# Optimization experiments

Hardware: AMD Instinct MI355X
Metric: run time of the kernel (lower is better)

## Reference

```python
import jax, jax.numpy as jnp
import numpy as np

N, E = 100000, 1600000
IN_C, HID, OUT_C, EDGE_D, GRAPH_D = 32, 32, 8, 16, 16

def _lin_w(key, fan_in, fan_out):
    return jax.random.normal(key, (fan_in, fan_out), dtype=jnp.float32) * (1.0 / np.sqrt(fan_in))

def setup_inputs() -> dict:
    key = jax.random.key(0)
    ks = jax.random.split(key, 12)
    return {
        "x": jax.random.uniform(ks[0], (N, IN_C), dtype=jnp.float32),
        "edge_attr": jax.random.uniform(ks[1], (E, EDGE_D), dtype=jnp.float32),
        "graph_attr": jax.random.uniform(ks[2], (1, GRAPH_D), dtype=jnp.float32),
        "edge_index": jax.random.randint(ks[3], (2, E), 0, N, dtype=jnp.int32),
        "batch": jnp.zeros((N,), dtype=jnp.int32),
        "W_node": _lin_w(ks[4], IN_C, HID),
        "b_node": jnp.zeros((HID,), jnp.float32),
        "W_graph": _lin_w(ks[5], GRAPH_D, GRAPH_D),
        "b_graph": jnp.zeros((GRAPH_D,), jnp.float32),
        "W_edge_agg": _lin_w(ks[6], 2 * HID + EDGE_D + GRAPH_D, EDGE_D),
        "b_edge_agg": jnp.zeros((EDGE_D,), jnp.float32),
        "W_node_agg": _lin_w(ks[7], EDGE_D + HID + GRAPH_D, HID),
        "b_node_agg": jnp.zeros((HID,), jnp.float32),
        "W_sage_l": _lin_w(ks[8], HID, OUT_C),
        "b_sage_l": jnp.zeros((OUT_C,), jnp.float32),
        "W_sage_r": _lin_w(ks[9], HID, OUT_C),
    }

def _seg_mean(vals, idx, num_segments):
    # scatter-mean: sum per segment / count (count clamped to 1 for empty segments)
    sums = jax.ops.segment_sum(vals, idx, num_segments=num_segments)
    cnt = jax.ops.segment_sum(jnp.ones((vals.shape[0],), vals.dtype), idx, num_segments=num_segments)
    return sums / jnp.maximum(cnt, 1.0)[:, None]

def reference(x, edge_attr, graph_attr, edge_index, batch,
              W_node, b_node, W_graph, b_graph,
              W_edge_agg, b_edge_agg, W_node_agg, b_node_agg,
              W_sage_l, b_sage_l, W_sage_r):
    n = x.shape[0]
    row, col = edge_index[0], edge_index[1]
    # node / graph embeddings (plain linear, no activation)
    h_i = x @ W_node + b_node                       # [N, HID]
    h_G = graph_attr @ W_graph + b_graph            # [1, GRAPH_D]
    h_G_e = jnp.broadcast_to(h_G, (row.shape[0], h_G.shape[1]))
    # edge aggregator: gather both endpoints, concat, linear, relu
    edge_in = jnp.concatenate([h_i[row], h_i[col], edge_attr, h_G_e], axis=-1)  # [E, 96]
    h_edge_agg = jax.nn.relu(edge_in @ W_edge_agg + b_edge_agg)                 # [E, EDGE_D]
    # per-node mean of edges whose source == node (replaces O(N*E) python loop)
    m_N = _seg_mean(h_edge_agg, row, n)             # [N, EDGE_D]
    # node aggregator
    h_G_n = jnp.broadcast_to(h_G, (n, h_G.shape[1]))
    h_i2 = jax.nn.relu(jnp.concatenate([h_i, m_N, h_G_n], axis=-1) @ W_node_agg + b_node_agg)
    # SAGEConv (mean aggr): out = lin_l(mean_{j->i} x_j) + lin_r(x_i)
    agg = _seg_mean(h_i2[row], col, n)
    h_nodes = agg @ W_sage_l + b_sage_l + h_i2 @ W_sage_r  # [N, OUT_C]
    # global mean pool over batch assignment (single graph here)
    pooled = _seg_mean(h_nodes, batch, 1)           # [1, OUT_C]
    return jax.nn.log_softmax(pooled, axis=1)
```

## Files before the change

### kernel.cpp

```cpp
#include <hip/hip_runtime.h>
#include <hip/hip_fp16.h>
#include <hip/hip_fp8.h>

#define HID 32
#define IN_C 32
#define EDGE_D 16
#define GRAPH_D 16
#define OUT_C 8
#define STRIDE 48

__device__ __forceinline__ unsigned char f32_to_fp8(float f) {
    __hip_fp8_e4m3 v(f);
    return (unsigned char)v.__x;
}
__device__ __forceinline__ float fp8_to_f32(unsigned char b) {
    __hip_fp8_e4m3 v;
    v.__x = (__hip_fp8_storage_t)b;
    return (float)v;
}

__global__ void __launch_bounds__(256)
k_node_emb(const float* __restrict__ x,
           const float* __restrict__ W,
           const float* __restrict__ b,
           const float* __restrict__ graph_attr,
           const float* __restrict__ W_graph,
           const float* __restrict__ b_graph,
           const float* __restrict__ W_edge_agg,
           const float* __restrict__ b_edge_agg,
           const float* __restrict__ W_node_agg,
           const float* __restrict__ b_node_agg,
           float* __restrict__ bias_edge,
           float* __restrict__ bias_node,
           int* __restrict__ zero_base, int zero_count,
           __half* __restrict__ h,
           unsigned char* __restrict__ Pr,
           unsigned char* __restrict__ Pc, int n) {
    __shared__ float hG[GRAPH_D];
    int t = threadIdx.x;
    for (int idx = blockIdx.x * blockDim.x + t; idx < zero_count;
         idx += gridDim.x * blockDim.x)
        zero_base[idx] = 0;

    if (blockIdx.x == 0 && t < GRAPH_D) {
        float acc = b_graph[t];
        for (int d = 0; d < GRAPH_D; d++)
            acc += graph_attr[d] * W_graph[d * GRAPH_D + t];
        hG[t] = acc;
    }
    __syncthreads();
    if (blockIdx.x == 0) {
        if (t < EDGE_D) {
            float acc = b_edge_agg[t];
            for (int d = 0; d < GRAPH_D; d++)
                acc += hG[d] * W_edge_agg[(2 * HID + EDGE_D + d) * EDGE_D + t];
            bias_edge[t] = acc;
        }
        if (t < HID) {
            float acc = b_node_agg[t];
            for (int d = 0; d < GRAPH_D; d++)
                acc += hG[d] * W_node_agg[(HID + EDGE_D + d) * HID + t];
            bias_node[t] = acc;
        }
    }

    int i = blockIdx.x * blockDim.x + t;
    if (i >= n) return;
    float in[IN_C];
    const float4* xr = (const float4*)(x + (size_t)i * IN_C);
#pragma unroll
    for (int q = 0; q < IN_C / 4; q++) {
        float4 v = xr[q];
        in[4 * q + 0] = v.x; in[4 * q + 1] = v.y;
        in[4 * q + 2] = v.z; in[4 * q + 3] = v.w;
    }
    float acc[HID];
#pragma unroll
    for (int j = 0; j < HID; j++) acc[j] = b[j];
#pragma unroll
    for (int k = 0; k < IN_C; k++) {
        float a = in[k];
#pragma unroll
        for (int j = 0; j < HID; j++) acc[j] += a * W[k * HID + j];
    }
    float4 packed[4];
    __half2* ph = (__half2*)packed;
#pragma unroll
    for (int j = 0; j < 16; j++)
        ph[j] = __floats2half2_rn(acc[2 * j], acc[2 * j + 1]);
    float4* hr = (float4*)(h + (size_t)i * HID);
#pragma unroll
    for (int q = 0; q < 4; q++) hr[q] = packed[q];

    float pr[EDGE_D], pc[EDGE_D];
#pragma unroll
    for (int j = 0; j < EDGE_D; j++) { pr[j] = 0.f; pc[j] = 0.f; }
#pragma unroll
    for (int k = 0; k < HID; k++) {
        float a = acc[k];
#pragma unroll
        for (int j = 0; j < EDGE_D; j++) {
            pr[j] += a * W_edge_agg[k * EDGE_D + j];
            pc[j] += a * W_edge_agg[(HID + k) * EDGE_D + j];
        }
    }
    unsigned char pb[EDGE_D];
#pragma unroll
    for (int j = 0; j < EDGE_D; j++) pb[j] = f32_to_fp8(pr[j]);
    *(uint4*)(Pr + (size_t)i * EDGE_D) = *(const uint4*)pb;
#pragma unroll
    for (int j = 0; j < EDGE_D; j++) pb[j] = f32_to_fp8(pc[j]);
    *(uint4*)(Pc + (size_t)i * EDGE_D) = *(const uint4*)pb;
}

__global__ void __launch_bounds__(256)
k_edge_place(const int* __restrict__ ei,
             const unsigned char* __restrict__ Pr,
             const unsigned char* __restrict__ Pc,
             const float* __restrict__ ea,
             const float* __restrict__ We,
             const float* __restrict__ biasE,
             int* __restrict__ cur_row,
             int* __restrict__ cur_col,
             __half* __restrict__ he_bucket, int E) {
    int e = blockIdx.x * blockDim.x + threadIdx.x;
    if (e >= E) return;
    int r = ei[e];
    int c = ei[E + e];

    uint4 g = *(const uint4*)(Pr + (size_t)r * EDGE_D);
    uint4 q = *(const uint4*)(Pc + (size_t)c * EDGE_D);
    float eav[EDGE_D];
    {
        const float4* er = (const float4*)(ea + (size_t)e * EDGE_D);
#pragma unroll
        for (int k = 0; k < 4; k++) {
            float4 v = er[k];
            eav[4 * k + 0] = v.x; eav[4 * k + 1] = v.y;
            eav[4 * k + 2] = v.z; eav[4 * k + 3] = v.w;
        }
    }
    int pr = atomicAdd(cur_row + r, 1);
    atomicAdd(cur_col + c, 1);

    float acc[EDGE_D];
    {
        const unsigned char* gb = (const unsigned char*)&g;
        const unsigned char* qb = (const unsigned char*)&q;
#pragma unroll
        for (int j = 0; j < EDGE_D; j++)
            acc[j] = biasE[j] + fp8_to_f32(gb[j]) + fp8_to_f32(qb[j]);
    }
#pragma unroll
    for (int k = 0; k < EDGE_D; k++) {
        float a = eav[k];
#pragma unroll
        for (int j = 0; j < EDGE_D; j++)
            acc[j] += a * We[(2 * HID + k) * EDGE_D + j];
    }

    if (pr < STRIDE) {
        float4 packed[2];
        __half2* ph = (__half2*)packed;
#pragma unroll
        for (int j = 0; j < 8; j++)
            ph[j] = __floats2half2_rn(fmaxf(acc[2 * j], 0.f),
                                      fmaxf(acc[2 * j + 1], 0.f));
        float4* dst = (float4*)(he_bucket + ((size_t)r * STRIDE + pr) * EDGE_D);
        dst[0] = packed[0];
        dst[1] = packed[1];
    }
}

#define RNODES 128
__global__ void __launch_bounds__(256)
k_reduce(const __half* __restrict__ hi,
         const __half* __restrict__ he_bucket,
         const int* __restrict__ cur_row,
         const int* __restrict__ batch,
         const float* __restrict__ Wna,
         const float* __restrict__ Wsl,
         const float* __restrict__ Wsr,
         const float* __restrict__ biasN,
         __half* __restrict__ zout,
         float* __restrict__ pool,
         float* __restrict__ ncnt, int n) {
    __shared__ float ms_s[RNODES][EDGE_D + 1];
    __shared__ int cnt_s[RNODES];
    __shared__ float red[4][OUT_C + 1];
    __shared__ float redc[4];
    int tid = threadIdx.x;
    int g = tid >> 4;
    int l = tid & 15;
    int base = blockIdx.x * RNODES;

    if (tid < RNODES)
        cnt_s[tid] = (base + tid < n) ? cur_row[base + tid] : 0;
    __syncthreads();

    for (int iter = 0; iter < RNODES / 16; iter++) {
        int node = base + iter * 16 + g;
        int cnt = cnt_s[iter * 16 + g];
        int d = cnt < STRIDE ? cnt : STRIDE;
        float inv = 1.0f / fmaxf((float)cnt, 1.0f);
        float a16[EDGE_D];
#pragma unroll
        for (int j = 0; j < EDGE_D; j++) a16[j] = 0.f;
        const __half* bb = he_bucket + (size_t)node * STRIDE * EDGE_D;
        for (int t = l; t < d; t += 16) {
            const float4* rp = (const float4*)(bb + t * EDGE_D);
            float4 lo = rp[0], hi4 = rp[1];
            const __half2* hp0 = (const __half2*)&lo;
            const __half2* hp1 = (const __half2*)&hi4;
#pragma unroll
            for (int j = 0; j < 4; j++) {
                float2 f0 = __half22float2(hp0[j]);
                float2 f1 = __half22float2(hp1[j]);
                a16[2 * j]     += f0.x; a16[2 * j + 1] += f0.y;
                a16[8 + 2 * j] += f1.x; a16[8 + 2 * j + 1] += f1.y;
            }
        }
#pragma unroll
        for (int m = 8; m >= 1; m >>= 1) {
#pragma unroll
            for (int k = 0; k < m; k++) {
                float send = (l & m) ? a16[k] : a16[k + m];
                float recv = __shfl_xor(send, m, 16);
                float keep = (l & m) ? a16[k + m] : a16[k];
                a16[k] = keep + recv;
            }
        }
        ms_s[iter * 16 + g][l] = a16[0] * inv;
    }
    __syncthreads();

    int i = base + tid;
    float rvv[OUT_C];
#pragma unroll
    for (int j = 0; j < OUT_C; j++) rvv[j] = 0.f;
    float cc = 0.f;

    if (tid < RNODES && i < n) {
        float ms[EDGE_D];
#pragma unroll
        for (int k = 0; k < EDGE_D; k++) ms[k] = ms_s[tid][k];

        float hr[HID];
        {
            float4 t[4];
            const float4* hrow = (const float4*)(hi + (size_t)i * HID);
#pragma unroll
            for (int q = 0; q < 4; q++) t[q] = hrow[q];
            const __half2* hp = (const __half2*)t;
#pragma unroll
            for (int j = 0; j < 16; j++) {
                float2 f = __half22float2(hp[j]);
                hr[2 * j] = f.x; hr[2 * j + 1] = f.y;
            }
        }
        float h2[HID];
#pragma unroll
        for (int j = 0; j < HID; j++) h2[j] = biasN[j];
#pragma unroll
        for (int k = 0; k < HID; k++) {
            float a = hr[k];
#pragma unroll
            for (int j = 0; j < HID; j++) h2[j] += a * Wna[k * HID + j];
        }
#pragma unroll
        for (int k = 0; k < EDGE_D; k++) {
            float a = ms[k];
#pragma unroll
            for (int j = 0; j < HID; j++) h2[j] += a * Wna[(HID + k) * HID + j];
        }
#pragma unroll
        for (int j = 0; j < HID; j++) h2[j] = fmaxf(h2[j], 0.f);

        float zv[OUT_C];
#pragma unroll
        for (int j = 0; j < OUT_C; j++) zv[j] = 0.f;
#pragma unroll
        for (int k = 0; k < HID; k++) {
            float a = h2[k];
#pragma unroll
            for (int j = 0; j < OUT_C; j++) {
                zv[j]  += a * Wsl[k * OUT_C + j];
                rvv[j] += a * Wsr[k * OUT_C + j];
            }
        }
        float4 packed;
        __half2* ph = (__half2*)&packed;
#pragma unroll
        for (int j = 0; j < 4; j++)
            ph[j] = __floats2half2_rn(zv[2 * j], zv[2 * j + 1]);
        *(float4*)(zout + (size_t)i * OUT_C) = packed;
        if (batch[i] == 0) cc = 1.f; else {
#pragma unroll
            for (int j = 0; j < OUT_C; j++) rvv[j] = 0.f;
        }
    }
#pragma unroll
    for (int off = 32; off > 0; off >>= 1) {
#pragma unroll
        for (int j = 0; j < OUT_C; j++) rvv[j] += __shfl_down(rvv[j], off, 64);
        cc += __shfl_down(cc, off, 64);
    }
    int w = tid >> 6;
    if ((tid & 63) == 0) {
#pragma unroll
        for (int j = 0; j < OUT_C; j++) red[w][j] = rvv[j];
        redc[w] = cc;
    }
    __syncthreads();
    if (tid < OUT_C) {
        float s = red[0][tid] + red[1][tid] + red[2][tid] + red[3][tid];
        atomicAdd(pool + tid, s);
    }
    if (tid == OUT_C) {
        atomicAdd(ncnt, redc[0] + redc[1] + redc[2] + redc[3]);
    }
}

#define POOL_BLOCKS 1280
__global__ void __launch_bounds__(256)
k_pool(const int* __restrict__ ei,
       const __half* __restrict__ z,
       const int* __restrict__ cur_col,
       float* __restrict__ pool, int E) {
    __shared__ float red[4][OUT_C + 1];
    int tid = threadIdx.x;
    float w8[OUT_C];
#pragma unroll
    for (int j = 0; j < OUT_C; j++) w8[j] = 0.f;
    for (int e = blockIdx.x * blockDim.x + tid; e < E;
         e += gridDim.x * blockDim.x) {
        int r = ei[e];
        int c = ei[E + e];
        float inv = 1.0f / fmaxf((float)cur_col[c], 1.0f);
        float4 t = *(const float4*)(z + (size_t)r * OUT_C);
        const __half2* hp = (const __half2*)&t;
#pragma unroll
        for (int j = 0; j < 4; j++) {
            float2 f = __half22float2(hp[j]);
            w8[2 * j]     += f.x * inv;
            w8[2 * j + 1] += f.y * inv;
        }
    }
#pragma unroll
    for (int off = 32; off > 0; off >>= 1) {
#pragma unroll
        for (int j = 0; j < OUT_C; j++) w8[j] += __shfl_down(w8[j], off, 64);
    }
    int w = tid >> 6;
    if ((tid & 63) == 0) {
#pragma unroll
        for (int j = 0; j < OUT_C; j++) red[w][j] = w8[j];
    }
    __syncthreads();
    if (tid < OUT_C) {
        float s = red[0][tid] + red[1][tid] + red[2][tid] + red[3][tid];
        atomicAdd(pool + tid, s);
    }
}

__global__ void k_final(const float* __restrict__ pool,
                        const float* __restrict__ ncnt,
                        const float* __restrict__ bsl,
                        float* __restrict__ out) {
    if (threadIdx.x == 0 && blockIdx.x == 0) {
        float c = fmaxf(ncnt[0], 1.0f);
        float p[OUT_C];
        float m = -1e30f;
#pragma unroll
        for (int j = 0; j < OUT_C; j++) {
            p[j] = pool[j] / c + bsl[j];
            m = fmaxf(m, p[j]);
        }
        float s = 0.f;
#pragma unroll
        for (int j = 0; j < OUT_C; j++) s += expf(p[j] - m);
        float l = logf(s);
#pragma unroll
        for (int j = 0; j < OUT_C; j++) out[j] = p[j] - m - l;
    }
}

extern "C" void kernel_launch(void* const* d_in, const int* in_sizes, int n_in,
                              void* d_out, int out_size, void* d_ws, size_t ws_size,
                              hipStream_t stream) {
    const float* x          = (const float*)d_in[0];
    const float* edge_attr  = (const float*)d_in[1];
    const float* graph_attr = (const float*)d_in[2];
    const int*   edge_index = (const int*)d_in[3];
    const int*   batch      = (const int*)d_in[4];
    const float* W_node     = (const float*)d_in[5];
    const float* b_node     = (const float*)d_in[6];
    const float* W_graph    = (const float*)d_in[7];
    const float* b_graph    = (const float*)d_in[8];
    const float* W_edge_agg = (const float*)d_in[9];
    const float* b_edge_agg = (const float*)d_in[10];
    const float* W_node_agg = (const float*)d_in[11];
    const float* b_node_agg = (const float*)d_in[12];
    const float* W_sage_l   = (const float*)d_in[13];
    const float* b_sage_l   = (const float*)d_in[14];
    const float* W_sage_r   = (const float*)d_in[15];

    const int n = in_sizes[0] / IN_C;
    const int E = in_sizes[3] / 2;

    char* wsb = (char*)d_ws;
    int*  cur_row = (int*)wsb;
    int*  cur_col = cur_row + n;
    float* pool   = (float*)(cur_col + n);
    float* ncnt   = pool + 8;
    int   zero_count = 2 * n + 16;
    size_t off = (size_t)zero_count * 4;
    __half* he_bucket = (__half*)(wsb + off); off += (size_t)n * STRIDE * EDGE_D * 2;
    __half* h_i  = (__half*)(wsb + off); off += (size_t)n * HID * 2;
    __half* zarr = (__half*)(wsb + off); off += (size_t)n * OUT_C * 2;
    float* biasE = (float*)(wsb + off);  off += 16 * 4;
    float* biasN = (float*)(wsb + off);  off += HID * 4;
    unsigned char* Pr = (unsigned char*)(wsb + off); off += (size_t)n * EDGE_D;
    unsigned char* Pc = (unsigned char*)(wsb + off); off += (size_t)n * EDGE_D;

    k_node_emb<<<(n + 255) / 256, 256, 0, stream>>>(x, W_node, b_node,
                                                    graph_attr, W_graph, b_graph,
                                                    W_edge_agg, b_edge_agg,
                                                    W_node_agg, b_node_agg,
                                                    biasE, biasN,
                                                    cur_row, zero_count, h_i,
                                                    Pr, Pc, n);

    k_edge_place<<<(E + 255) / 256, 256, 0, stream>>>(edge_index, Pr, Pc, edge_attr,
                                                      W_edge_agg, biasE,
                                                      cur_row, cur_col,
                                                      he_bucket, E);

    k_reduce<<<(n + RNODES - 1) / RNODES, 256, 0, stream>>>(h_i, he_bucket, cur_row,
                                                            batch, W_node_agg,
                                                            W_sage_l, W_sage_r,
                                                            biasN, zarr, pool, ncnt, n);

    k_pool<<<POOL_BLOCKS, 256, 0, stream>>>(edge_index, zarr, cur_col, pool, E);

    k_final<<<1, 64, 0, stream>>>(pool, ncnt, b_sage_l, (float*)d_out);
}
```

Baseline: 459.9 us.

## Fold SAGE pooling into reduce via per-node weighted sums, drop edge pool pass

Uses linearity of the final mean pool to replace the per-edge k_pool pass. Each node's hidden vector is weighted by the sum of 1/indeg(col) over its outgoing edges, taken from the column index now stored in each bucket slot, and accumulated into global 32-wide vectors. The SAGE linear layers are then applied once in k_final. Bucket entries switch from fp16 to fp8 values plus a stored column index in 32-byte slots. This removes a full edge sweep and the z array, at the cost of fp8 precision loss, a random cur_col gather in the reduce kernel, and heavier shuffle reductions.

Result: slower. 503.9 us (+9.6%).

```diff
diff --git a/kernel.cpp b/kernel.cpp
--- a/kernel.cpp
+++ b/kernel.cpp
@@ -8,6 +8,7 @@
 #define GRAPH_D 16
 #define OUT_C 8
 #define STRIDE 48
+#define SLOT_B 32
 
 __device__ __forceinline__ unsigned char f32_to_fp8(float f) {
     __hip_fp8_e4m3 v(f);
@@ -122,7 +123,7 @@
              const float* __restrict__ biasE,
              int* __restrict__ cur_row,
              int* __restrict__ cur_col,
-             __half* __restrict__ he_bucket, int E) {
+             unsigned char* __restrict__ he_bucket, int E) {
     int e = blockIdx.x * blockDim.x + threadIdx.x;
     if (e >= E) return;
     int r = ei[e];
@@ -160,34 +161,35 @@
     }
 
     if (pr < STRIDE) {
-        float4 packed[2];
-        __half2* ph = (__half2*)packed;
-#pragma unroll
-        for (int j = 0; j < 8; j++)
-            ph[j] = __floats2half2_rn(fmaxf(acc[2 * j], 0.f),
-                                      fmaxf(acc[2 * j + 1], 0.f));
-        float4* dst = (float4*)(he_bucket + ((size_t)r * STRIDE + pr) * EDGE_D);
-        dst[0] = packed[0];
-        dst[1] = packed[1];
+        unsigned char hb[16];
+#pragma unroll
+        for (int j = 0; j < EDGE_D; j++)
+            hb[j] = f32_to_fp8(fmaxf(acc[j], 0.f));
+        uint4 w0 = *(const uint4*)hb;
+        uint4 w1; w1.x = (unsigned int)c; w1.y = 0; w1.z = 0; w1.w = 0;
+        unsigned char* dst = he_bucket + ((size_t)r * STRIDE + pr) * SLOT_B;
+        *(uint4*)dst = w0;
+        *(uint4*)(dst + 16) = w1;
     }
 }
 
 #define RNODES 128
 __global__ void __launch_bounds__(256)
 k_reduce(const __half* __restrict__ hi,
-         const __half* __restrict__ he_bucket,
+         const unsigned char* __restrict__ he_bucket,
          const int* __restrict__ cur_row,
+         const int* __restrict__ cur_col,
          const int* __restrict__ batch,
          const float* __restrict__ Wna,
-         const float* __restrict__ Wsl,
-         const float* __restrict__ Wsr,
          const float* __restrict__ biasN,
-         __half* __restrict__ zout,
-         float* __restrict__ pool,
+         float* __restrict__ Vg,
+         float* __restrict__ Wg,
          float* __restrict__ ncnt, int n) {
     __shared__ float ms_s[RNODES][EDGE_D + 1];
+    __shared__ float s_s[RNODES];
     __shared__ int cnt_s[RNODES];
-    __shared__ float red[4][OUT_C + 1];
+    __shared__ float vpart[4][HID];
+    __shared__ float wpart[4][HID];
     __shared__ float redc[4];
     int tid = threadIdx.x;
     int g = tid >> 4;
@@ -206,19 +208,17 @@
         float a16[EDGE_D];
 #pragma unroll
         for (int j = 0; j < EDGE_D; j++) a16[j] = 0.f;
-        const __half* bb = he_bucket + (size_t)node * STRIDE * EDGE_D;
+        float sw = 0.f;
+        const unsigned char* bb = he_bucket + (size_t)node * STRIDE * SLOT_B;
         for (int t = l; t < d; t += 16) {
-            const float4* rp = (const float4*)(bb + t * EDGE_D);
-            float4 lo = rp[0], hi4 = rp[1];
-            const __half2* hp0 = (const __half2*)&lo;
-            const __half2* hp1 = (const __half2*)&hi4;
-#pragma unroll
-            for (int j = 0; j < 4; j++) {
-                float2 f0 = __half22float2(hp0[j]);
-                float2 f1 = __half22float2(hp1[j]);
-                a16[2 * j]     += f0.x; a16[2 * j + 1] += f0.y;
-                a16[8 + 2 * j] += f1.x; a16[8 + 2 * j + 1] += f1.y;
-            }
+            uint4 q0 = *(const uint4*)(bb + (size_t)t * SLOT_B);
+            int col = *(const int*)(bb + (size_t)t * SLOT_B + 16);
+            int ic = cur_col[col];
+            sw += 1.0f / fmaxf((float)ic, 1.0f);
+            const unsigned char* qb = (const unsigned char*)&q0;
+#pragma unroll
+            for (int j = 0; j < EDGE_D; j++)
+                a16[j] += fp8_to_f32(qb[j]);
         }
 #pragma unroll
         for (int m = 8; m >= 1; m >>= 1) {
@@ -230,20 +230,25 @@
                 a16[k] = keep + recv;
             }
         }
+#pragma unroll
+        for (int m = 1; m <= 8; m <<= 1) sw += __shfl_xor(sw, m, 16);
         ms_s[iter * 16 + g][l] = a16[0] * inv;
+        if (l == 0) s_s[iter * 16 + g] = sw;
     }
     __syncthreads();
 
     int i = base + tid;
-    float rvv[OUT_C];
-#pragma unroll
-    for (int j = 0; j < OUT_C; j++) rvv[j] = 0.f;
+    float vv[HID];
+    float h2[HID];
+#pragma unroll
+    for (int j = 0; j < HID; j++) { vv[j] = 0.f; h2[j] = 0.f; }
     float cc = 0.f;
 
     if (tid < RNODES && i < n) {
         float ms[EDGE_D];
 #pragma unroll
         for (int k = 0; k < EDGE_D; k++) ms[k] = ms_s[tid][k];
+        float sv = s_s[tid];
 
         float hr[HID];
         {
@@ -258,7 +263,6 @@
                 hr[2 * j] = f.x; hr[2 * j + 1] = f.y;
             }
         }
-        float h2[HID];
 #pragma unroll
         for (int j = 0; j < HID; j++) h2[j] = biasN[j];
 #pragma unroll
@@ -276,95 +280,64 @@
 #pragma unroll
         for (int j = 0; j < HID; j++) h2[j] = fmaxf(h2[j], 0.f);
 
-        float zv[OUT_C];
-#pragma unroll
-        for (int j = 0; j < OUT_C; j++) zv[j] = 0.f;
-#pragma unroll
-        for (int k = 0; k < HID; k++) {
-            float a = h2[k];
-#pragma unroll
-            for (int j = 0; j < OUT_C; j++) {
-                zv[j]  += a * Wsl[k * OUT_C + j];
-                rvv[j] += a * Wsr[k * OUT_C + j];
+#pragma unroll
+        for (int j = 0; j < HID; j++) vv[j] = sv * h2[j];
+
+        if (batch[i] == 0) cc = 1.f;
+        else {
+#pragma unroll
+            for (int j = 0; j < HID; j++) h2[j] = 0.f;
+        }
+    }
+
+#pragma unroll
+    for (int k = 0; k < HID; k++) {
+        vv[k] += __shfl_xor(vv[k], 32, 64);
+        h2[k] += __shfl_xor(h2[k], 32, 64);
+    }
+    int l32 = tid & 31;
+#pragma unroll
+    for (int m = 16; m >= 1; m >>= 1) {
+#pragma unroll
+        for (int k = 0; k < m; k++) {
+            {
+                float send = (l32 & m) ? vv[k] : vv[k + m];
+                float recv = __shfl_xor(send, m, 32);
+                float keep = (l32 & m) ? vv[k + m] : vv[k];
+                vv[k] = keep + recv;
             }
-        }
-        float4 packed;
-        __half2* ph = (__half2*)&packed;
-#pragma unroll
-        for (int j = 0; j < 4; j++)
-            ph[j] = __floats2half2_rn(zv[2 * j], zv[2 * j + 1]);
-        *(float4*)(zout + (size_t)i * OUT_C) = packed;
-        if (batch[i] == 0) cc = 1.f; else {
-#pragma unroll
-            for (int j = 0; j < OUT_C; j++) rvv[j] = 0.f;
-        }
-    }
-#pragma unroll
-    for (int off = 32; off > 0; off >>= 1) {
-#pragma unroll
-        for (int j = 0; j < OUT_C; j++) rvv[j] += __shfl_down(rvv[j], off, 64);
-        cc += __shfl_down(cc, off, 64);
+            {
+                float send = (l32 & m) ? h2[k] : h2[k + m];
+                float recv = __shfl_xor(send, m, 32);
+                float keep = (l32 & m) ? h2[k + m] : h2[k];
+                h2[k] = keep + recv;
+            }
+        }
     }
     int w = tid >> 6;
-    if ((tid & 63) == 0) {
-#pragma unroll
-        for (int j = 0; j < OUT_C; j++) red[w][j] = rvv[j];
-        redc[w] = cc;
-    }
+    if ((tid & 63) < 32) {
+        vpart[w][l32] = vv[0];
+        wpart[w][l32] = h2[0];
+    }
+#pragma unroll
+    for (int off = 32; off > 0; off >>= 1) cc += __shfl_down(cc, off, 64);
+    if ((tid & 63) == 0) redc[w] = cc;
     __syncthreads();
-    if (tid < OUT_C) {
-        float s = red[0][tid] + red[1][tid] + red[2][tid] + red[3][tid];
-        atomicAdd(pool + tid, s);
-    }
-    if (tid == OUT_C) {
+    if (tid < HID) {
+        atomicAdd(Vg + tid, vpart[0][tid] + vpart[1][tid] + vpart[2][tid] + vpart[3][tid]);
+    } else if (tid < 2 * HID) {
+        int j = tid - HID;
+        atomicAdd(Wg + j, wpart[0][j] + wpart[1][j] + wpart[2][j] + wpart[3][j]);
+    } else if (tid == 2 * HID) {
         atomicAdd(ncnt, redc[0] + redc[1] + redc[2] + redc[3]);
     }
 }
 
-#define POOL_BLOCKS 1280
-__global__ void __launch_bounds__(256)
-k_pool(const int* __restrict__ ei,
-       const __half* __restrict__ z,
-       const int* __restrict__ cur_col,
-       float* __restrict__ pool, int E) {
-    __shared__ float red[4][OUT_C + 1];
-    int tid = threadIdx.x;
-    float w8[OUT_C];
-#pragma unroll
-    for (int j = 0; j < OUT_C; j++) w8[j] = 0.f;
-    for (int e = blockIdx.x * blockDim.x + tid; e < E;
-         e += gridDim.x * blockDim.x) {
-        int r = ei[e];
-        int c = ei[E + e];
-        float inv = 1.0f / fmaxf((float)cur_col[c], 1.0f);
-        float4 t = *(const float4*)(z + (size_t)r * OUT_C);
-        const __half2* hp = (const __half2*)&t;
-#pragma unroll
-        for (int j = 0; j < 4; j++) {
-            float2 f = __half22float2(hp[j]);
-            w8[2 * j]     += f.x * inv;
-            w8[2 * j + 1] += f.y * inv;
-        }
-    }
-#pragma unroll
-    for (int off = 32; off > 0; off >>= 1) {
-#pragma unroll
-        for (int j = 0; j < OUT_C; j++) w8[j] += __shfl_down(w8[j], off, 64);
-    }
-    int w = tid >> 6;
-    if ((tid & 63) == 0) {
-#pragma unroll
-        for (int j = 0; j < OUT_C; j++) red[w][j] = w8[j];
-    }
-    __syncthreads();
-    if (tid < OUT_C) {
-        float s = red[0][tid] + red[1][tid] + red[2][tid] + red[3][tid];
-        atomicAdd(pool + tid, s);
-    }
-}
-
-__global__ void k_final(const float* __restrict__ pool,
+__global__ void k_final(const float* __restrict__ Vg,
+                        const float* __restrict__ Wg,
                         const float* __restrict__ ncnt,
+                        const float* __restrict__ Wsl,
+                        const float* __restrict__ Wsr,
                         const float* __restrict__ bsl,
                         float* __restrict__ out) {
     if (threadIdx.x == 0 && blockIdx.x == 0) {
@@ -372,8 +345,16 @@
         float p[OUT_C];
         float m = -1e30f;
 #pragma unroll
+        for (int j = 0; j < OUT_C; j++) p[j] = 0.f;
+        for (int k = 0; k < HID; k++) {
+            float v = Vg[k], w = Wg[k];
+#pragma unroll
+            for (int j = 0; j < OUT_C; j++)
+                p[j] += v * Wsl[k * OUT_C + j] + w * Wsr[k * OUT_C + j];
+        }
+#pragma unroll
         for (int j = 0; j < OUT_C; j++) {
-            p[j] = pool[j] / c + bsl[j];
+            p[j] = p[j] / c + bsl[j];
             m = fmaxf(m, p[j]);
         }
         float s = 0.f;
@@ -411,13 +392,14 @@
     char* wsb = (char*)d_ws;
     int*  cur_row = (int*)wsb;
     int*  cur_col = cur_row + n;
-    float* pool   = (float*)(cur_col + n);
-    float* ncnt   = pool + 8;
-    int   zero_count = 2 * n + 16;
+    float* Vg     = (float*)(cur_col + n);
+    float* Wg     = Vg + HID;
+    float* ncnt   = Wg + HID;
+    int   zero_count = 2 * n + 80;
     size_t off = (size_t)zero_count * 4;
-    __half* he_bucket = (__half*)(wsb + off); off += (size_t)n * STRIDE * EDGE_D * 2;
+    unsigned char* he_bucket = (unsigned char*)(wsb + off);
+    off += (size_t)n * STRIDE * SLOT_B;
     __half* h_i  = (__half*)(wsb + off); off += (size_t)n * HID * 2;
-    __half* zarr = (__half*)(wsb + off); off += (size_t)n * OUT_C * 2;
     float* biasE = (float*)(wsb + off);  off += 16 * 4;
     float* biasN = (float*)(wsb + off);  off += HID * 4;
     unsigned char* Pr = (unsigned char*)(wsb + off); off += (size_t)n * EDGE_D;
@@ -436,12 +418,11 @@
                                                       cur_row, cur_col,
                                                       he_bucket, E);
 
-    k_reduce<<<(n + RNODES - 1) / RNODES, 256, 0, stream>>>(h_i, he_bucket, cur_row,
+    k_reduce<<<(n + RNODES - 1) / RNODES, 256, 0, stream>>>(h_i, he_bucket,
+                                                            cur_row, cur_col,
                                                             batch, W_node_agg,
-                                                            W_sage_l, W_sage_r,
-                                                            biasN, zarr, pool, ncnt, n);
-
-    k_pool<<<POOL_BLOCKS, 256, 0, stream>>>(edge_index, zarr, cur_col, pool, E);
-
-    k_final<<<1, 64, 0, stream>>>(pool, ncnt, b_sage_l, (float*)d_out);
-}
+                                                            biasN, Vg, Wg, ncnt, n);
+
+    k_final<<<1, 64, 0, stream>>>(Vg, Wg, ncnt, W_sage_l, W_sage_r,
+                                  b_sage_l, (float*)d_out);
+}
```

## Store edge buckets in fp8, precompute node-agg projection, grid-stride edge placement with prefetch

Applied to the files above, without the earlier changes.

Edge bucket entries are now stored as 16 fp8 bytes instead of 32 fp16 bytes, halving scatter-write and reduce-read traffic. The h_i part of the node aggregator matmul (h_i @ W_node_agg[:HID]) is moved into the node embedding kernel, so the reduce kernel reads a precomputed projection and skips that 32x32 product. Edge placement becomes a grid-stride loop over a capped number of blocks that prefetches the next edge's indices and Pr/Pc gathers to hide latency. The change trades precision: fp8 edge activations add quantisation error to the mean.

Result: slower. 538.7 us (+17.1%).

```diff
diff --git a/kernel.cpp b/kernel.cpp
--- a/kernel.cpp
+++ b/kernel.cpp
@@ -33,7 +33,7 @@
            float* __restrict__ bias_edge,
            float* __restrict__ bias_node,
            int* __restrict__ zero_base, int zero_count,
-           __half* __restrict__ h,
+           __half* __restrict__ An,
            unsigned char* __restrict__ Pr,
            unsigned char* __restrict__ Pc, int n) {
     __shared__ float hG[GRAPH_D];
@@ -83,36 +83,51 @@
 #pragma unroll
         for (int j = 0; j < HID; j++) acc[j] += a * W[k * HID + j];
     }
-    float4 packed[4];
-    __half2* ph = (__half2*)packed;
-#pragma unroll
-    for (int j = 0; j < 16; j++)
-        ph[j] = __floats2half2_rn(acc[2 * j], acc[2 * j + 1]);
-    float4* hr = (float4*)(h + (size_t)i * HID);
-#pragma unroll
-    for (int q = 0; q < 4; q++) hr[q] = packed[q];
-
-    float pr[EDGE_D], pc[EDGE_D];
-#pragma unroll
-    for (int j = 0; j < EDGE_D; j++) { pr[j] = 0.f; pc[j] = 0.f; }
-#pragma unroll
-    for (int k = 0; k < HID; k++) {
-        float a = acc[k];
-#pragma unroll
-        for (int j = 0; j < EDGE_D; j++) {
-            pr[j] += a * W_edge_agg[k * EDGE_D + j];
-            pc[j] += a * W_edge_agg[(HID + k) * EDGE_D + j];
-        }
-    }
-    unsigned char pb[EDGE_D];
-#pragma unroll
-    for (int j = 0; j < EDGE_D; j++) pb[j] = f32_to_fp8(pr[j]);
-    *(uint4*)(Pr + (size_t)i * EDGE_D) = *(const uint4*)pb;
-#pragma unroll
-    for (int j = 0; j < EDGE_D; j++) pb[j] = f32_to_fp8(pc[j]);
-    *(uint4*)(Pc + (size_t)i * EDGE_D) = *(const uint4*)pb;
-}
-
+
+    {
+        float pr[EDGE_D], pc[EDGE_D];
+#pragma unroll
+        for (int j = 0; j < EDGE_D; j++) { pr[j] = 0.f; pc[j] = 0.f; }
+#pragma unroll
+        for (int k = 0; k < HID; k++) {
+            float a = acc[k];
+#pragma unroll
+            for (int j = 0; j < EDGE_D; j++) {
+                pr[j] += a * W_edge_agg[k * EDGE_D + j];
+                pc[j] += a * W_edge_agg[(HID + k) * EDGE_D + j];
+            }
+        }
+        unsigned char pb[EDGE_D];
+#pragma unroll
+        for (int j = 0; j < EDGE_D; j++) pb[j] = f32_to_fp8(pr[j]);
+        *(uint4*)(Pr + (size_t)i * EDGE_D) = *(const uint4*)pb;
+#pragma unroll
+        for (int j = 0; j < EDGE_D; j++) pb[j] = f32_to_fp8(pc[j]);
+        *(uint4*)(Pc + (size_t)i * EDGE_D) = *(const uint4*)pb;
+    }
+
+    {
+        float an[HID];
+#pragma unroll
+        for (int j = 0; j < HID; j++) an[j] = 0.f;
+#pragma unroll
+        for (int k = 0; k < HID; k++) {
+            float a = acc[k];
+#pragma unroll
+            for (int j = 0; j < HID; j++) an[j] += a * W_node_agg[k * HID + j];
+        }
+        float4 packed[4];
+        __half2* ph = (__half2*)packed;
+#pragma unroll
+        for (int j = 0; j < 16; j++)
+            ph[j] = __floats2half2_rn(an[2 * j], an[2 * j + 1]);
+        float4* dst = (float4*)(An + (size_t)i * HID);
+#pragma unroll
+        for (int q = 0; q < 4; q++) dst[q] = packed[q];
+    }
+}
+
+#define EPLACE_BLOCKS 2048
 __global__ void __launch_bounds__(256)
 k_edge_place(const int* __restrict__ ei,
              const unsigned char* __restrict__ Pr,
@@ -122,60 +137,75 @@
              const float* __restrict__ biasE,
              int* __restrict__ cur_row,
              int* __restrict__ cur_col,
-             __half* __restrict__ he_bucket, int E) {
+             unsigned char* __restrict__ he_bucket, int E) {
+    const int stride = gridDim.x * blockDim.x;
     int e = blockIdx.x * blockDim.x + threadIdx.x;
     if (e >= E) return;
+
+    float bE[EDGE_D];
+#pragma unroll
+    for (int j = 0; j < EDGE_D; j++) bE[j] = biasE[j];
+
     int r = ei[e];
     int c = ei[E + e];
-
     uint4 g = *(const uint4*)(Pr + (size_t)r * EDGE_D);
     uint4 q = *(const uint4*)(Pc + (size_t)c * EDGE_D);
-    float eav[EDGE_D];
-    {
-        const float4* er = (const float4*)(ea + (size_t)e * EDGE_D);
-#pragma unroll
-        for (int k = 0; k < 4; k++) {
-            float4 v = er[k];
-            eav[4 * k + 0] = v.x; eav[4 * k + 1] = v.y;
-            eav[4 * k + 2] = v.z; eav[4 * k + 3] = v.w;
-        }
-    }
-    int pr = atomicAdd(cur_row + r, 1);
-    atomicAdd(cur_col + c, 1);
-
-    float acc[EDGE_D];
-    {
-        const unsigned char* gb = (const unsigned char*)&g;
-        const unsigned char* qb = (const unsigned char*)&q;
-#pragma unroll
-        for (int j = 0; j < EDGE_D; j++)
-            acc[j] = biasE[j] + fp8_to_f32(gb[j]) + fp8_to_f32(qb[j]);
-    }
-#pragma unroll
-    for (int k = 0; k < EDGE_D; k++) {
-        float a = eav[k];
-#pragma unroll
-        for (int j = 0; j < EDGE_D; j++)
-            acc[j] += a * We[(2 * HID + k) * EDGE_D + j];
-    }
-
-    if (pr < STRIDE) {
-        float4 packed[2];
-        __half2* ph = (__half2*)packed;
-#pragma unroll
-        for (int j = 0; j < 8; j++)
-            ph[j] = __floats2half2_rn(fmaxf(acc[2 * j], 0.f),
-                                      fmaxf(acc[2 * j + 1], 0.f));
-        float4* dst = (float4*)(he_bucket + ((size_t)r * STRIDE + pr) * EDGE_D);
-        dst[0] = packed[0];
-        dst[1] = packed[1];
+
+    while (true) {
+        int e2 = e + stride;
+        int rn = r, cn = c;
+        uint4 gn = g, qn = q;
+        if (e2 < E) {
+            rn = ei[e2];
+            cn = ei[E + e2];
+            gn = *(const uint4*)(Pr + (size_t)rn * EDGE_D);
+            qn = *(const uint4*)(Pc + (size_t)cn * EDGE_D);
+        }
+        float eav[EDGE_D];
+        {
+            const float4* er = (const float4*)(ea + (size_t)e * EDGE_D);
+#pragma unroll
+            for (int k = 0; k < 4; k++) {
+                float4 v = er[k];
+                eav[4 * k + 0] = v.x; eav[4 * k + 1] = v.y;
+                eav[4 * k + 2] = v.z; eav[4 * k + 3] = v.w;
+            }
+        }
+        int pr = atomicAdd(cur_row + r, 1);
+        atomicAdd(cur_col + c, 1);
+
+        float acc[EDGE_D];
+        {
+            const unsigned char* gb = (const unsigned char*)&g;
+            const unsigned char* qb = (const unsigned char*)&q;
+#pragma unroll
+            for (int j = 0; j < EDGE_D; j++)
+                acc[j] = bE[j] + fp8_to_f32(gb[j]) + fp8_to_f32(qb[j]);
+        }
+#pragma unroll
+        for (int k = 0; k < EDGE_D; k++) {
+            float a = eav[k];
+#pragma unroll
+            for (int j = 0; j < EDGE_D; j++)
+                acc[j] += a * We[(2 * HID + k) * EDGE_D + j];
+        }
+        if (pr < STRIDE) {
+            unsigned char hb[EDGE_D];
+#pragma unroll
+            for (int j = 0; j < EDGE_D; j++)
+                hb[j] = f32_to_fp8(fmaxf(acc[j], 0.f));
+            *(uint4*)(he_bucket + ((size_t)r * STRIDE + pr) * EDGE_D) =
+                *(const uint4*)hb;
+        }
+        if (e2 >= E) break;
+        e = e2; r = rn; c = cn; g = gn; q = qn;
     }
 }
 
 #define RNODES 128
 __global__ void __launch_bounds__(256)
-k_reduce(const __half* __restrict__ hi,
-         const __half* __restrict__ he_bucket,
+k_reduce(const __half* __restrict__ An,
+         const unsigned char* __restrict__ he_bucket,
          const int* __restrict__ cur_row,
          const int* __restrict__ batch,
          const float* __restrict__ Wna,
@@ -206,19 +236,13 @@
         float a16[EDGE_D];
 #pragma unroll
         for (int j = 0; j < EDGE_D; j++) a16[j] = 0.f;
-        const __half* bb = he_bucket + (size_t)node * STRIDE * EDGE_D;
+        const unsigned char* bb = he_bucket + (size_t)node * STRIDE * EDGE_D;
         for (int t = l; t < d; t += 16) {
-            const float4* rp = (const float4*)(bb + t * EDGE_D);
-            float4 lo = rp[0], hi4 = rp[1];
-            const __half2* hp0 = (const __half2*)&lo;
-            const __half2* hp1 = (const __half2*)&hi4;
-#pragma unroll
-            for (int j = 0; j < 4; j++) {
-                float2 f0 = __half22float2(hp0[j]);
-                float2 f1 = __half22float2(hp1[j]);
-                a16[2 * j]     += f0.x; a16[2 * j + 1] += f0.y;
-                a16[8 + 2 * j] += f1.x; a16[8 + 2 * j + 1] += f1.y;
-            }
+            uint4 q0 = *(const uint4*)(bb + (size_t)t * EDGE_D);
+            const unsigned char* qb = (const unsigned char*)&q0;
+#pragma unroll
+            for (int j = 0; j < EDGE_D; j++)
+                a16[j] += fp8_to_f32(qb[j]);
         }
 #pragma unroll
         for (int m = 8; m >= 1; m >>= 1) {
@@ -241,37 +265,26 @@
     float cc = 0.f;
 
     if (tid < RNODES && i < n) {
-        float ms[EDGE_D];
-#pragma unroll
-        for (int k = 0; k < EDGE_D; k++) ms[k] = ms_s[tid][k];
-
-        float hr[HID];
+        float h2[HID];
         {
-            float4 t[4];
-            const float4* hrow = (const float4*)(hi + (size_t)i * HID);
-#pragma unroll
-            for (int q = 0; q < 4; q++) t[q] = hrow[q];
-            const __half2* hp = (const __half2*)t;
+            float4 t4[4];
+            const float4* arow = (const float4*)(An + (size_t)i * HID);
+#pragma unroll
+            for (int q = 0; q < 4; q++) t4[q] = arow[q];
+            const __half2* hp = (const __half2*)t4;
 #pragma unroll
             for (int j = 0; j < 16; j++) {
                 float2 f = __half22float2(hp[j]);
-                hr[2 * j] = f.x; hr[2 * j + 1] = f.y;
+                h2[2 * j]     = f.x + biasN[2 * j];
+                h2[2 * j + 1] = f.y + biasN[2 * j + 1];
             }
         }
-        float h2[HID];
-#pragma unroll
-        for (int j = 0; j < HID; j++) h2[j] = biasN[j];
-#pragma unroll
-        for (int k = 0; k < HID; k++) {
-            float a = hr[k];
-#pragma unroll
-            for (int j = 0; j < HID; j++) h2[j] += a * Wna[k * HID + j];
-        }
 #pragma unroll
         for (int k = 0; k < EDGE_D; k++) {
-            float a = ms[k];
-#pragma unroll
-            for (int j = 0; j < HID; j++) h2[j] += a * Wna[(HID + k) * HID + j];
+            float a = ms_s[tid][k];
+#pragma unroll
+            for (int j = 0; j < HID; j++)
+                h2[j] += a * Wna[(HID + k) * HID + j];
         }
 #pragma unroll
         for (int j = 0; j < HID; j++) h2[j] = fmaxf(h2[j], 0.f);
@@ -415,8 +428,9 @@
     float* ncnt   = pool + 8;
     int   zero_count = 2 * n + 16;
     size_t off = (size_t)zero_count * 4;
-    __half* he_bucket = (__half*)(wsb + off); off += (size_t)n * STRIDE * EDGE_D * 2;
-    __half* h_i  = (__half*)(wsb + off); off += (size_t)n * HID * 2;
+    unsigned char* he_bucket = (unsigned char*)(wsb + off);
+    off += (size_t)n * STRIDE * EDGE_D;
+    __half* An   = (__half*)(wsb + off); off += (size_t)n * HID * 2;
     __half* zarr = (__half*)(wsb + off); off += (size_t)n * OUT_C * 2;
     float* biasE = (float*)(wsb + off);  off += 16 * 4;
     float* biasN = (float*)(wsb + off);  off += HID * 4;
@@ -428,18 +442,22 @@
                                                     W_edge_agg, b_edge_agg,
                                                     W_node_agg, b_node_agg,
                                                     biasE, biasN,
-                                                    cur_row, zero_count, h_i,
+                                                    cur_row, zero_count, An,
                                                     Pr, Pc, n);
 
-    k_edge_place<<<(E + 255) / 256, 256, 0, stream>>>(edge_index, Pr, Pc, edge_attr,
-                                                      W_edge_agg, biasE,
-                                                      cur_row, cur_col,
-                                                      he_bucket, E);
-
-    k_reduce<<<(n + RNODES - 1) / RNODES, 256, 0, stream>>>(h_i, he_bucket, cur_row,
-                                                            batch, W_node_agg,
+    int eblk = (E + 255) / 256;
+    if (eblk > EPLACE_BLOCKS) eblk = EPLACE_BLOCKS;
+    k_edge_place<<<eblk, 256, 0, stream>>>(edge_index, Pr, Pc, edge_attr,
+                                           W_edge_agg, biasE,
+                                           cur_row, cur_col,
+                                           he_bucket, E);
+
+    k_reduce<<<(n + RNODES - 1) / RNODES, 256, 0, stream>>>(An, he_bucket,
+                                                            cur_row, batch,
+                                                            W_node_agg,
                                                             W_sage_l, W_sage_r,
-                                                            biasN, zarr, pool, ncnt, n);
+                                                            biasN, zarr,
+                                                            pool, ncnt, n);
 
     k_pool<<<POOL_BLOCKS, 256, 0, stream>>>(edge_index, zarr, cur_col, pool, E);
 
```
